# Performance work log

Hardware: AMD Instinct MI355X
Metric: run time of the kernel (lower is better)

Reference implementation:

```python
import jax, jax.numpy as jnp
import numpy as np

N_NODES = 50000

def _lgconv(x, src, dst, norm):
    # gather-scale-scatter: out[i] = sum_{(j->i)} norm_e * x[j]
    msgs = x[src] * norm[:, None]                      # [E, d]
    return jax.ops.segment_sum(msgs, dst, num_segments=N_NODES)  # [N, d]

def setup_inputs() -> dict:
    key = jax.random.key(0)
    k1, k2 = jax.random.split(key)
    x = jax.random.normal(k1, (N_NODES, 128), dtype=jnp.float32)
    edge_index = jax.random.randint(k2, (2, 600000), 0, N_NODES, dtype=jnp.int64)
    return {"x": x, "edge_index": edge_index}

def reference(x, edge_index):
    src, dst = edge_index[0], edge_index[1]
    # PyG gcn_norm (no self loops, edge_weight = 1):
    deg = jax.ops.segment_sum(jnp.ones_like(src, dtype=x.dtype), dst, num_segments=N_NODES)
    dinv = jnp.where(deg > 0, jax.lax.rsqrt(jnp.where(deg > 0, deg, 1.0)), 0.0)
    norm = dinv[src] * dinv[dst]                       # [E]
    # Three stacked LGConv + relu (dropout is identity in eval mode)
    x = jax.nn.relu(_lgconv(x, src, dst, norm))
    x = jax.nn.relu(_lgconv(x, src, dst, norm))
    x = jax.nn.relu(_lgconv(x, src, dst, norm))
    return x
```

## Files before the change

### kernel.cpp

```cpp
#include <hip/hip_runtime.h>
#include <hip/hip_fp16.h>

#define NN 50000
#define FEAT 128
#define CSTRIDE 16

__global__ void init_kernel(const unsigned int* ei32, int* flag, int* hist, int n) {
    int i = blockIdx.x * 256 + threadIdx.x;
    if (i < n) hist[i] = 0;
    if (blockIdx.x == 0) {
        __shared__ int ok;
        if (threadIdx.x == 0) ok = 1;
        __syncthreads();
        if (ei32[2 * threadIdx.x + 1] != 0u) ok = 0;
        __syncthreads();
        if (threadIdx.x == 0) *flag = ok;
    }
}

static __device__ __forceinline__ void load_edge(const void* ei, int is64, int E, int e,
                                                 int& src, int& dst) {
    if (is64) {
        const long long* p = (const long long*)ei;
        src = (int)p[e];
        dst = (int)p[E + e];
    } else {
        const int* p = (const int*)ei;
        src = p[e];
        dst = p[E + e];
    }
}

__global__ void hist_kernel(const void* ei, const int* flag, int* hist, int E) {
    int base = (blockIdx.x * blockDim.x + threadIdx.x) * 4;
    if (base >= E) return;
    const int is64 = *flag;
    int n = E - base; if (n > 4) n = 4;
    int src[4], dst[4];
    #pragma unroll
    for (int i = 0; i < 4; ++i)
        if (i < n) load_edge(ei, is64, E, base + i, src[i], dst[i]);
    #pragma unroll
    for (int i = 0; i < 4; ++i)
        if (i < n) atomicAdd(&hist[dst[i]], 1);
}

__global__ void scan_local_kernel(const int* __restrict__ hist, int* __restrict__ local_excl,
                                  int* __restrict__ bsum, float* __restrict__ dinv, int n) {
    __shared__ int sdata[256];
    int i = blockIdx.x * 256 + threadIdx.x;
    int v = (i < n) ? hist[i] : 0;
    if (i < n) dinv[i] = (v > 0) ? rsqrtf((float)v) : 0.0f;
    sdata[threadIdx.x] = v;
    __syncthreads();
    for (int d = 1; d < 256; d <<= 1) {
        int t = (threadIdx.x >= (unsigned)d) ? sdata[threadIdx.x - d] : 0;
        __syncthreads();
        sdata[threadIdx.x] += t;
        __syncthreads();
    }
    if (i < n) local_excl[i] = sdata[threadIdx.x] - v;
    if (threadIdx.x == 255) bsum[blockIdx.x] = sdata[255];
}

__global__ void scan_bsum_kernel(int* bsum, int nb) {
    __shared__ int sdata[1024];
    int v = ((int)threadIdx.x < nb) ? bsum[threadIdx.x] : 0;
    sdata[threadIdx.x] = v;
    __syncthreads();
    for (int d = 1; d < 1024; d <<= 1) {
        int t = (threadIdx.x >= (unsigned)d) ? sdata[threadIdx.x - d] : 0;
        __syncthreads();
        sdata[threadIdx.x] += t;
        __syncthreads();
    }
    if ((int)threadIdx.x < nb) bsum[threadIdx.x] = sdata[threadIdx.x] - v;
}

__global__ void scan_add_kernel(const int* __restrict__ local_excl, const int* __restrict__ bsum,
                                int* __restrict__ rowp, int* __restrict__ curs, int n, int E) {
    int i = blockIdx.x * 256 + threadIdx.x;
    if (i < n) {
        int r = local_excl[i] + bsum[i >> 8];
        rowp[i] = r;
        curs[i * CSTRIDE] = r;
    }
    if (i == 0) rowp[n] = E;
}

__global__ void scatter_kernel(const void* ei, const int* flag, int* cursor,
                               int* __restrict__ col, int E) {
    int base = (blockIdx.x * blockDim.x + threadIdx.x) * 4;
    if (base >= E) return;
    const int is64 = *flag;
    int n = E - base; if (n > 4) n = 4;

    int src[4], dst[4];
    #pragma unroll
    for (int i = 0; i < 4; ++i)
        if (i < n) load_edge(ei, is64, E, base + i, src[i], dst[i]);

    int pos[4];
    #pragma unroll
    for (int i = 0; i < 4; ++i)
        if (i < n) pos[i] = atomicAdd(&cursor[dst[i] * CSTRIDE], 1);

    #pragma unroll
    for (int i = 0; i < 4; ++i)
        if (i < n) col[pos[i]] = src[i];
}

static __device__ __forceinline__ float4 relu4(float4 v) {
    v.x = fmaxf(v.x, 0.0f); v.y = fmaxf(v.y, 0.0f);
    v.z = fmaxf(v.z, 0.0f); v.w = fmaxf(v.w, 0.0f);
    return v;
}

static __device__ __forceinline__ void fma4(float4& a, float w, float4 v) {
    a.x += w * v.x; a.y += w * v.y; a.z += w * v.z; a.w += w * v.w;
}

static __device__ __forceinline__ float4 h4_to_f4(uint2 r) {
    __half2 lo = *reinterpret_cast<__half2*>(&r.x);
    __half2 hi = *reinterpret_cast<__half2*>(&r.y);
    float2 f0 = __half22float2(lo);
    float2 f1 = __half22float2(hi);
    return make_float4(f0.x, f0.y, f1.x, f1.y);
}

static __device__ __forceinline__ uint2 f4_to_h4(float4 v) {
    __half2 lo = __floats2half2_rn(v.x, v.y);
    __half2 hi = __floats2half2_rn(v.z, v.w);
    uint2 r;
    r.x = *reinterpret_cast<unsigned int*>(&lo);
    r.y = *reinterpret_cast<unsigned int*>(&hi);
    return r;
}

__global__ void cvt_f2h_kernel(const float4* __restrict__ in, const float* __restrict__ dinv,
                               uint2* __restrict__ outh, int n4) {
    int i = blockIdx.x * blockDim.x + threadIdx.x;
    if (i >= n4) return;
    float dd = dinv[i >> 5];
    float4 v = in[i];
    v.x *= dd; v.y *= dd; v.z *= dd; v.w *= dd;
    outh[i] = f4_to_h4(v);
}

template <bool OUT_HALF>
__global__ void conv_h_kernel(const uint2* __restrict__ xh,
                              const int* __restrict__ row_ptr,
                              const int* __restrict__ col,
                              const float* __restrict__ dinv,
                              void* __restrict__ outbuf) {
    int gid = blockIdx.x * blockDim.x + threadIdx.x;
    int node = gid >> 5;
    int f4   = gid & 31;
    if (node >= NN) return;
    int beg = row_ptr[node];
    int end = row_ptr[node + 1];
    float dd = dinv[node];

    float4 a0 = make_float4(0.f, 0.f, 0.f, 0.f);
    float4 a1 = a0, a2 = a0, a3 = a0;

    for (int cb = beg; cb < end; cb += 32) {
        int rem = end - cb;
        if (rem > 32) rem = 32;
        int myi = (f4 < rem) ? f4 : 0;
        int pk = col[cb + myi];

        for (int j = 0; j < rem; j += 8) {
            int i0 = j + 0, i1 = j + 1, i2 = j + 2, i3 = j + 3;
            int i4 = j + 4, i5 = j + 5, i6 = j + 6, i7 = j + 7;
            int last = rem - 1;
            int c0 = __shfl(pk, i0 < rem ? i0 : last, 32);
            int c1 = __shfl(pk, i1 < rem ? i1 : last, 32);
            int c2 = __shfl(pk, i2 < rem ? i2 : last, 32);
            int c3 = __shfl(pk, i3 < rem ? i3 : last, 32);
            int c4 = __shfl(pk, i4 < rem ? i4 : last, 32);
            int c5 = __shfl(pk, i5 < rem ? i5 : last, 32);
            int c6 = __shfl(pk, i6 < rem ? i6 : last, 32);
            int c7 = __shfl(pk, i7 < rem ? i7 : last, 32);

            float w0 = (i0 < rem) ? 1.0f : 0.0f;
            float w1 = (i1 < rem) ? 1.0f : 0.0f;
            float w2 = (i2 < rem) ? 1.0f : 0.0f;
            float w3 = (i3 < rem) ? 1.0f : 0.0f;
            float w4 = (i4 < rem) ? 1.0f : 0.0f;
            float w5 = (i5 < rem) ? 1.0f : 0.0f;
            float w6 = (i6 < rem) ? 1.0f : 0.0f;
            float w7 = (i7 < rem) ? 1.0f : 0.0f;

            uint2 r0 = xh[c0 * 32 + f4];
            uint2 r1 = xh[c1 * 32 + f4];
            uint2 r2 = xh[c2 * 32 + f4];
            uint2 r3 = xh[c3 * 32 + f4];
            uint2 r4 = xh[c4 * 32 + f4];
            uint2 r5 = xh[c5 * 32 + f4];
            uint2 r6 = xh[c6 * 32 + f4];
            uint2 r7 = xh[c7 * 32 + f4];

            fma4(a0, w0, h4_to_f4(r0));
            fma4(a1, w1, h4_to_f4(r1));
            fma4(a2, w2, h4_to_f4(r2));
            fma4(a3, w3, h4_to_f4(r3));
            fma4(a0, w4, h4_to_f4(r4));
            fma4(a1, w5, h4_to_f4(r5));
            fma4(a2, w6, h4_to_f4(r6));
            fma4(a3, w7, h4_to_f4(r7));
        }
    }

    float4 acc;
    acc.x = (a0.x + a1.x) + (a2.x + a3.x);
    acc.y = (a0.y + a1.y) + (a2.y + a3.y);
    acc.z = (a0.z + a1.z) + (a2.z + a3.z);
    acc.w = (a0.w + a1.w) + (a2.w + a3.w);
    acc.x *= dd; acc.y *= dd; acc.z *= dd; acc.w *= dd;
    acc = relu4(acc);

    if (OUT_HALF) {
        acc.x *= dd; acc.y *= dd; acc.z *= dd; acc.w *= dd;
        ((uint2*)outbuf)[node * 32 + f4] = f4_to_h4(acc);
    } else {
        ((float4*)outbuf)[node * 32 + f4] = acc;
    }
}

__global__ void deg_kernel(const void* ei, const int* flag, float* deg, int E) {
    int e = blockIdx.x * blockDim.x + threadIdx.x;
    if (e >= E) return;
    int src, dst;
    load_edge(ei, *flag, E, e, src, dst);
    atomicAdd(&deg[dst], 1.0f);
}

__global__ void dinv_kernel(float* deg) {
    int i = blockIdx.x * blockDim.x + threadIdx.x;
    if (i >= NN) return;
    float d = deg[i];
    deg[i] = (d > 0.0f) ? (1.0f / sqrtf(d)) : 0.0f;
}

template <bool RELU_IN>
__global__ void conv_atomic_kernel(const float* __restrict__ xin, const void* ei, const int* flag,
                                   const float* __restrict__ dinv, float* __restrict__ yout, int E) {
    int gid = blockIdx.x * blockDim.x + threadIdx.x;
    int e  = gid >> 5;
    int f4 = gid & 31;
    if (e >= E) return;
    int src, dst;
    load_edge(ei, *flag, E, e, src, dst);
    float w = dinv[src] * dinv[dst];
    float4 v = ((const float4*)xin)[src * 32 + f4];
    if (RELU_IN) v = relu4(v);
    float* o = yout + (size_t)dst * FEAT + f4 * 4;
    atomicAdd(o + 0, v.x * w);
    atomicAdd(o + 1, v.y * w);
    atomicAdd(o + 2, v.z * w);
    atomicAdd(o + 3, v.w * w);
}

__global__ void relu_kernel(float4* buf, int n4) {
    int i = blockIdx.x * blockDim.x + threadIdx.x;
    if (i >= n4) return;
    buf[i] = relu4(buf[i]);
}

extern "C" void kernel_launch(void* const* d_in, const int* in_sizes, int n_in,
                              void* d_out, int out_size, void* d_ws, size_t ws_size,
                              hipStream_t stream) {
    const float* x  = (const float*)d_in[0];
    const void*  ei = d_in[1];
    const int E = in_sizes[1] / 2;

    float* out = (float*)d_out;
    char*  ws  = (char*)d_ws;

    const size_t feat_bytes  = (size_t)NN * FEAT * sizeof(float);
    const size_t half_bytes  = (size_t)NN * FEAT * sizeof(unsigned short);
    const int NB = (NN + 255) / 256;
    const int N4 = NN * 32;

    const size_t OFF_FLAG = 0;
    const size_t OFF_HIST = 1024;
    const size_t OFF_DINV = OFF_HIST + (((size_t)NN * 4 + 255) & ~255ull);
    const size_t OFF_ROWP = OFF_DINV + (((size_t)NN * 4 + 255) & ~255ull);
    const size_t OFF_CURS = OFF_ROWP + ((((size_t)NN + 1) * 4 + 255) & ~255ull);
    const size_t OFF_BSUM = OFF_CURS + (((size_t)NN * 4 * CSTRIDE + 255) & ~255ull);
    const size_t OFF_EDG  = OFF_BSUM + ((1024 * 4 + 255) & ~255ull);
    const size_t OFF_HA   = OFF_EDG + (((size_t)E * 4 + 255) & ~255ull);
    const size_t OFF_HB   = OFF_HA + ((half_bytes + 255) & ~255ull);
    const size_t NEEDED   = OFF_HB + half_bytes;

    int* flag = (int*)(ws + OFF_FLAG);

    if (ws_size >= NEEDED) {
        int*   hist = (int*)(ws + OFF_HIST);
        float* dinv = (float*)(ws + OFF_DINV);
        int*   rowp = (int*)(ws + OFF_ROWP);
        int*   curs = (int*)(ws + OFF_CURS);
        int*   bsum = (int*)(ws + OFF_BSUM);
        int*   col  = (int*)(ws + OFF_EDG);
        uint2* hA   = (uint2*)(ws + OFF_HA);
        uint2* hB   = (uint2*)(ws + OFF_HB);

        init_kernel<<<NB, 256, 0, stream>>>((const unsigned int*)ei, flag, hist, NN);

        const int e4_blocks = (E / 4 + 255) / 256 + 1;
        hist_kernel<<<e4_blocks, 256, 0, stream>>>(ei, flag, hist, E);
        scan_local_kernel<<<NB, 256, 0, stream>>>(hist, rowp, bsum, dinv, NN);
        cvt_f2h_kernel<<<(N4 + 255) / 256, 256, 0, stream>>>((const float4*)x, dinv, hA, N4);
        scan_bsum_kernel<<<1, 1024, 0, stream>>>(bsum, NB);
        scan_add_kernel<<<NB, 256, 0, stream>>>(rowp, bsum, rowp, curs, NN, E);
        scatter_kernel<<<e4_blocks, 256, 0, stream>>>(ei, flag, curs, col, E);

        const int conv_blocks = (NN * 32 + 255) / 256;
        conv_h_kernel<true><<<conv_blocks, 256, 0, stream>>>(hA, rowp, col, dinv, hB);
        conv_h_kernel<true><<<conv_blocks, 256, 0, stream>>>(hB, rowp, col, dinv, hA);
        conv_h_kernel<false><<<conv_blocks, 256, 0, stream>>>(hA, rowp, col, dinv, out);
    } else {
        float* dinv = (float*)(ws + 1024);
        float* y    = (float*)(ws + 262144);

        hipMemsetAsync(dinv, 0, NN * sizeof(float), stream);
        hipMemsetAsync(out, 0, feat_bytes, stream);
        hipMemsetAsync(y, 0, feat_bytes, stream);

        init_kernel<<<1, 256, 0, stream>>>((const unsigned int*)ei, flag, (int*)(ws + 512), 256);
        deg_kernel<<<(E + 255) / 256, 256, 0, stream>>>(ei, flag, dinv, E);
        dinv_kernel<<<(NN + 255) / 256, 256, 0, stream>>>(dinv);

        const int conv_blocks = (int)(((size_t)E * 32 + 255) / 256);
        conv_atomic_kernel<false><<<conv_blocks, 256, 0, stream>>>(x, ei, flag, dinv, out, E);
        conv_atomic_kernel<true><<<conv_blocks, 256, 0, stream>>>(out, ei, flag, dinv, y, E);
        hipMemsetAsync(out, 0, feat_bytes, stream);
        conv_atomic_kernel<true><<<conv_blocks, 256, 0, stream>>>(y, ei, flag, dinv, out, E);
        relu_kernel<<<(out_size / 4 + 255) / 256, 256, 0, stream>>>((float4*)out, out_size / 4);
    }
}
```

Before: 149.5 us.

## Build CSR via atomic rank capture instead of second atomic scatter pass

The histogram kernel now records the value returned by each atomicAdd as the edge's rank within its destination row. The placement kernel then computes col positions as rowp[dst]+rank with no atomics, so the padded cursor array and the second round of contended atomics go away. This costs an extra E-sized rank buffer that must be written and read back. Col stores and loads are also marked nontemporal.

```diff
diff --git a/kernel.cpp b/kernel.cpp
--- a/kernel.cpp
+++ b/kernel.cpp
@@ -3,7 +3,6 @@
 
 #define NN 50000
 #define FEAT 128
-#define CSTRIDE 16
 
 __global__ void init_kernel(const unsigned int* ei32, int* flag, int* hist, int n) {
     int i = blockIdx.x * 256 + threadIdx.x;
@@ -31,7 +30,8 @@
     }
 }
 
-__global__ void hist_kernel(const void* ei, const int* flag, int* hist, int E) {
+__global__ void rank_kernel(const void* ei, const int* flag, int* hist,
+                            int* __restrict__ rank, int E) {
     int base = (blockIdx.x * blockDim.x + threadIdx.x) * 4;
     if (base >= E) return;
     const int is64 = *flag;
@@ -40,9 +40,13 @@
     #pragma unroll
     for (int i = 0; i < 4; ++i)
         if (i < n) load_edge(ei, is64, E, base + i, src[i], dst[i]);
-    #pragma unroll
-    for (int i = 0; i < 4; ++i)
-        if (i < n) atomicAdd(&hist[dst[i]], 1);
+    int r[4];
+    #pragma unroll
+    for (int i = 0; i < 4; ++i)
+        if (i < n) r[i] = atomicAdd(&hist[dst[i]], 1);
+    #pragma unroll
+    for (int i = 0; i < 4; ++i)
+        if (i < n) rank[base + i] = r[i];
 }
 
 __global__ void scan_local_kernel(const int* __restrict__ hist, int* __restrict__ local_excl,
@@ -78,36 +82,30 @@
 }
 
 __global__ void scan_add_kernel(const int* __restrict__ local_excl, const int* __restrict__ bsum,
-                                int* __restrict__ rowp, int* __restrict__ curs, int n, int E) {
+                                int* __restrict__ rowp, int n, int E) {
     int i = blockIdx.x * 256 + threadIdx.x;
-    if (i < n) {
-        int r = local_excl[i] + bsum[i >> 8];
-        rowp[i] = r;
-        curs[i * CSTRIDE] = r;
-    }
+    if (i < n) rowp[i] = local_excl[i] + bsum[i >> 8];
     if (i == 0) rowp[n] = E;
 }
 
-__global__ void scatter_kernel(const void* ei, const int* flag, int* cursor,
-                               int* __restrict__ col, int E) {
+__global__ void place_kernel(const void* ei, const int* flag,
+                             const int* __restrict__ rowp, const int* __restrict__ rank,
+                             int* __restrict__ col, int E) {
     int base = (blockIdx.x * blockDim.x + threadIdx.x) * 4;
     if (base >= E) return;
     const int is64 = *flag;
     int n = E - base; if (n > 4) n = 4;
-
-    int src[4], dst[4];
-    #pragma unroll
-    for (int i = 0; i < 4; ++i)
-        if (i < n) load_edge(ei, is64, E, base + i, src[i], dst[i]);
-
-    int pos[4];
-    #pragma unroll
-    for (int i = 0; i < 4; ++i)
-        if (i < n) pos[i] = atomicAdd(&cursor[dst[i] * CSTRIDE], 1);
-
-    #pragma unroll
-    for (int i = 0; i < 4; ++i)
-        if (i < n) col[pos[i]] = src[i];
+    int src[4], dst[4], r[4];
+    #pragma unroll
+    for (int i = 0; i < 4; ++i)
+        if (i < n) { load_edge(ei, is64, E, base + i, src[i], dst[i]); r[i] = rank[base + i]; }
+    int rp[4];
+    #pragma unroll
+    for (int i = 0; i < 4; ++i)
+        if (i < n) rp[i] = rowp[dst[i]];
+    #pragma unroll
+    for (int i = 0; i < 4; ++i)
+        if (i < n) __builtin_nontemporal_store(src[i], &col[rp[i] + r[i]]);
 }
 
 static __device__ __forceinline__ float4 relu4(float4 v) {
@@ -168,7 +166,7 @@
         int rem = end - cb;
         if (rem > 32) rem = 32;
         int myi = (f4 < rem) ? f4 : 0;
-        int pk = col[cb + myi];
+        int pk = __builtin_nontemporal_load(&col[cb + myi]);
 
         for (int j = 0; j < rem; j += 8) {
             int i0 = j + 0, i1 = j + 1, i2 = j + 2, i3 = j + 3;
@@ -287,10 +285,10 @@
     const size_t OFF_HIST = 1024;
     const size_t OFF_DINV = OFF_HIST + (((size_t)NN * 4 + 255) & ~255ull);
     const size_t OFF_ROWP = OFF_DINV + (((size_t)NN * 4 + 255) & ~255ull);
-    const size_t OFF_CURS = OFF_ROWP + ((((size_t)NN + 1) * 4 + 255) & ~255ull);
-    const size_t OFF_BSUM = OFF_CURS + (((size_t)NN * 4 * CSTRIDE + 255) & ~255ull);
-    const size_t OFF_EDG  = OFF_BSUM + ((1024 * 4 + 255) & ~255ull);
-    const size_t OFF_HA   = OFF_EDG + (((size_t)E * 4 + 255) & ~255ull);
+    const size_t OFF_BSUM = OFF_ROWP + ((((size_t)NN + 1) * 4 + 255) & ~255ull);
+    const size_t OFF_RNK  = OFF_BSUM + ((1024 * 4 + 255) & ~255ull);
+    const size_t OFF_COL  = OFF_RNK + (((size_t)E * 4 + 255) & ~255ull);
+    const size_t OFF_HA   = OFF_COL + (((size_t)E * 4 + 255) & ~255ull);
     const size_t OFF_HB   = OFF_HA + ((half_bytes + 255) & ~255ull);
     const size_t NEEDED   = OFF_HB + half_bytes;
 
@@ -300,21 +298,21 @@
         int*   hist = (int*)(ws + OFF_HIST);
         float* dinv = (float*)(ws + OFF_DINV);
         int*   rowp = (int*)(ws + OFF_ROWP);
-        int*   curs = (int*)(ws + OFF_CURS);
         int*   bsum = (int*)(ws + OFF_BSUM);
-        int*   col  = (int*)(ws + OFF_EDG);
+        int*   rank = (int*)(ws + OFF_RNK);
+        int*   col  = (int*)(ws + OFF_COL);
         uint2* hA   = (uint2*)(ws + OFF_HA);
         uint2* hB   = (uint2*)(ws + OFF_HB);
 
         init_kernel<<<NB, 256, 0, stream>>>((const unsigned int*)ei, flag, hist, NN);
 
         const int e4_blocks = (E / 4 + 255) / 256 + 1;
-        hist_kernel<<<e4_blocks, 256, 0, stream>>>(ei, flag, hist, E);
+        rank_kernel<<<e4_blocks, 256, 0, stream>>>(ei, flag, hist, rank, E);
         scan_local_kernel<<<NB, 256, 0, stream>>>(hist, rowp, bsum, dinv, NN);
         cvt_f2h_kernel<<<(N4 + 255) / 256, 256, 0, stream>>>((const float4*)x, dinv, hA, N4);
         scan_bsum_kernel<<<1, 1024, 0, stream>>>(bsum, NB);
-        scan_add_kernel<<<NB, 256, 0, stream>>>(rowp, bsum, rowp, curs, NN, E);
-        scatter_kernel<<<e4_blocks, 256, 0, stream>>>(ei, flag, curs, col, E);
+        scan_add_kernel<<<NB, 256, 0, stream>>>(rowp, bsum, rowp, NN, E);
+        place_kernel<<<e4_blocks, 256, 0, stream>>>(ei, flag, rowp, rank, col, E);
 
         const int conv_blocks = (NN * 32 + 255) / 256;
         conv_h_kernel<true><<<conv_blocks, 256, 0, stream>>>(hA, rowp, col, dinv, hB);
```

Measured after the change: 144.7 us. 1.03x faster.
